# Kernel optimization log

Hardware: AMD Instinct MI355X
Metric: run time of the kernel (lower is better)

Reference implementation:

```python
import jax, jax.numpy as jnp
import numpy as np

N_NODES = 100000
N_EDGES = 1600000
N_GRAPHS = 256
IN_F = 64   # global_features (GNN input dim)
OUT_F = 64  # node_features (GNN output dim)


def setup_inputs() -> dict:
    key = jax.random.key(0)
    ks = jax.random.split(key, 8)
    x = jax.random.normal(ks[0], (N_NODES, IN_F), dtype=jnp.float32)
    edge_index = jax.random.randint(ks[1], (2, N_EDGES), 0, N_NODES, dtype=jnp.int64)
    batch = jnp.sort(jax.random.randint(ks[2], (N_NODES,), 0, N_GRAPHS, dtype=jnp.int64))
    # GNNLayer linear: in=global_features, out=node_features
    W_gnn = jax.random.normal(ks[3], (IN_F, OUT_F), dtype=jnp.float32) / np.sqrt(IN_F)
    b_gnn = jnp.zeros((OUT_F,), dtype=jnp.float32)
    # global_attention: Linear(node_features, 1)
    W_att = jax.random.normal(ks[4], (OUT_F, 1), dtype=jnp.float32) / np.sqrt(OUT_F)
    b_att = jnp.zeros((1,), dtype=jnp.float32)
    return {"x": x, "edge_index": edge_index, "batch": batch,
            "W_gnn": W_gnn, "b_gnn": b_gnn, "W_att": W_att, "b_att": b_att}


def reference(x, edge_index, batch, W_gnn, b_gnn, W_att, b_att):
    src, dst = edge_index[0], edge_index[1]
    # --- GNN message passing layer: aggregate neighbor features, transform ---
    agg = jax.ops.segment_sum(x[src], dst, num_segments=N_NODES)  # [N, IN_F]
    h = jax.nn.relu((x + agg) @ W_gnn + b_gnn)                    # [N, OUT_F]
    # --- attention scores + scatter softmax over batch segments ---
    scores = (h @ W_att + b_att)[:, 0]                            # [N]
    seg_max = jax.ops.segment_max(scores, batch, num_segments=N_GRAPHS)
    e = jnp.exp(scores - seg_max[batch])
    denom = jax.ops.segment_sum(e, batch, num_segments=N_GRAPHS)
    w = e / denom[batch]                                          # [N]
    # --- weighted scatter-add pooling ---
    out = jax.ops.segment_sum(w[:, None] * h, batch, num_segments=N_GRAPHS)
    return out  # [N_GRAPHS, OUT_F]
```

## Files before the change

kernel.cpp:

```cpp
#include <hip/hip_runtime.h>

#define N_NODES  100000
#define N_EDGES  1600000
#define N_GRAPHS 256
#define F        64


#define CHUNK    8192
#define NCHUNK   196
#define NBUCK    391
#define BCAP     5120

#define CAST_ELEMS  (N_NODES * F / 4)
#define SC_BLOCKS   2000

__device__ __forceinline__ unsigned short f2bf(float f) {
    unsigned int u = __float_as_uint(f);
    u += 0x7FFFu + ((u >> 16) & 1u);
    return (unsigned short)(u >> 16);
}
__device__ __forceinline__ float bfl(unsigned int u) { return __uint_as_float(u << 16); }
__device__ __forceinline__ float bfh(unsigned int u) { return __uint_as_float(u & 0xFFFF0000u); }

__global__ __launch_bounds__(1024) void bin_kernel(
        const int* __restrict__ src, const int* __restrict__ dst,
        unsigned int* __restrict__ pairs, int* __restrict__ balloc) {
    __shared__ int hist[NBUCK];
    __shared__ int roffs[NBUCK];
    __shared__ int curs[NBUCK];
    __shared__ int bbase[NBUCK];
    __shared__ int wsum[16];
    __shared__ unsigned int   stage[CHUNK];
    __shared__ unsigned short bstage[CHUNK];

    int tid  = threadIdx.x;
    int b    = blockIdx.x;
    int base = b * CHUNK;
    int m    = min(CHUNK, N_EDGES - base);
    int lane = tid & 63;
    int wv   = tid >> 6;

    for (int k = tid; k < NBUCK; k += 1024) hist[k] = 0;
    __syncthreads();

    int de[8], se[8];
    #pragma unroll
    for (int r = 0; r < 8; ++r) {
        int e = tid + r * 1024;
        if (e < m) {
            de[r] = dst[base + e];
            se[r] = src[base + e];
            atomicAdd(&hist[de[r] >> 8], 1);
        } else {
            de[r] = -1; se[r] = 0;
        }
    }
    __syncthreads();

    int v = (tid < NBUCK) ? hist[tid] : 0;
    #pragma unroll
    for (int o = 1; o < 64; o <<= 1) {
        int u = __shfl_up(v, o, 64);
        if (lane >= o) v += u;
    }
    if (lane == 63) wsum[wv] = v;
    __syncthreads();
    if (tid < 16) {
        int s = wsum[tid];
        #pragma unroll
        for (int o = 1; o < 16; o <<= 1) {
            int u = __shfl_up(s, o, 64);
            if (tid >= o) s += u;
        }
        wsum[tid] = s;
    }
    __syncthreads();
    if (wv > 0) v += wsum[wv - 1];
    if (tid < NBUCK) {
        int excl = v - hist[tid];
        roffs[tid] = excl;
        curs[tid]  = excl;
        if (hist[tid] > 0)
            bbase[tid] = tid * BCAP + atomicAdd(&balloc[tid], hist[tid]);
    }
    __syncthreads();

    #pragma unroll
    for (int r = 0; r < 8; ++r) {
        if (de[r] >= 0) {
            int bk  = de[r] >> 8;
            int pos = atomicAdd(&curs[bk], 1);
            stage[pos]  = ((unsigned)(de[r] & 255) << 17) | (unsigned)se[r];
            bstage[pos] = (unsigned short)bk;
        }
    }
    __syncthreads();

    for (int e = tid; e < m; e += 1024) {
        int bk = bstage[e];
        pairs[bbase[bk] + (e - roffs[bk])] = stage[e];
    }
}

__global__ __launch_bounds__(512) void sortcast_kernel(
        unsigned int* __restrict__ pairs,
        const int* __restrict__ balloc,
        int* __restrict__ nbeg, int* __restrict__ nend,
        const float* __restrict__ x, unsigned short* __restrict__ xh,
        float* __restrict__ out, float* __restrict__ denom) {
    __shared__ int hist[256];
    __shared__ int roffs[256];
    __shared__ int curs[256];
    __shared__ int wsum[8];
    __shared__ int sorted[BCAP];

    int tid = threadIdx.x;
    int b   = blockIdx.x;

    if (b >= NBUCK) {
        if (b == NBUCK) {
            for (int i = tid; i < N_GRAPHS * F; i += 512) out[i] = 0.f;
            if (tid < N_GRAPHS) denom[tid] = 0.f;
        }
        int i0      = (b - NBUCK) * 512 + tid;
        int cstride = (SC_BLOCKS - NBUCK) * 512;
        for (int i = i0; i < CAST_ELEMS; i += cstride) {
            float4 v = ((const float4*)x)[i];
            ushort4 o;
            o.x = f2bf(v.x); o.y = f2bf(v.y); o.z = f2bf(v.z); o.w = f2bf(v.w);
            ((ushort4*)xh)[i] = o;
        }
        return;
    }

    int lane  = tid & 63;
    int wv    = tid >> 6;
    int node0 = b << 8;
    int nn    = min(256, N_NODES - node0);
    int E     = balloc[b];
    int base  = b * BCAP;

    for (int k = tid; k < 256; k += 512) hist[k] = 0;
    __syncthreads();
    for (int i = tid; i < E; i += 512)
        atomicAdd(&hist[pairs[base + i] >> 17], 1);
    __syncthreads();

    int c = (tid < 256) ? hist[tid] : 0;
    int v = c;
    #pragma unroll
    for (int o = 1; o < 64; o <<= 1) {
        int u = __shfl_up(v, o, 64);
        if (lane >= o) v += u;
    }
    if (tid < 256 && lane == 63) wsum[wv] = v;
    __syncthreads();
    if (tid < 4) {
        int s = wsum[tid];
        int u = __shfl_up(s, 1, 64); if (tid >= 1) s += u;
        u     = __shfl_up(s, 2, 64); if (tid >= 2) s += u;
        wsum[tid] = s;
    }
    __syncthreads();
    if (tid < 256) {
        if (wv > 0) v += wsum[wv - 1];
        int excl = v - c;
        roffs[tid] = excl;
        curs[tid]  = excl;
        if (tid < nn) {
            nbeg[node0 + tid] = base + excl;
            nend[node0 + tid] = base + excl + c;
        }
    }
    __syncthreads();

    for (int i = tid; i < E; i += 512) {
        unsigned int p = pairs[base + i];
        int pos = atomicAdd(&curs[p >> 17], 1);
        sorted[pos] = (int)(p & 0x1FFFFu);
    }
    __syncthreads();
    for (int i = tid; i < E; i += 512)
        pairs[base + i] = (unsigned int)sorted[i];
}

#define NODES_PER_WAVE 25
#define GT_NWAVES  (N_NODES / NODES_PER_WAVE)
#define GT_BLOCKS  (GT_NWAVES / 4)

__global__ __launch_bounds__(256) void gather_pool_kernel(
        const unsigned short* __restrict__ xh,
        const int*   __restrict__ nbeg,
        const int*   __restrict__ nend,
        const int*   __restrict__ eidx,
        const int*   __restrict__ batch,
        const float* __restrict__ Wg,
        const float* __restrict__ bg,
        const float* __restrict__ Wa,
        const float* __restrict__ ba,
        float*       __restrict__ out_acc,
        float*       __restrict__ denom) {
    int tid  = threadIdx.x;
    int lane = tid & 63;
    int grp  = lane >> 3;
    int c    = lane & 7;
    int waveId = blockIdx.x * 4 + (tid >> 6);

    int n0   = waveId * NODES_PER_WAVE;
    int nEnd = n0 + NODES_PER_WAVE;

    float wcol[F];
    #pragma unroll
    for (int k = 0; k < F; ++k) wcol[k] = Wg[k * F + lane];
    float bgl = bg[lane];
    float wal = Wa[lane];
    float ba0 = ba[0];

    const uint4* xh4 = (const uint4*)xh;

    int   cur_g = batch[n0];
    float accw  = 0.f;
    float denw  = 0.f;

    int pb = nbeg[n0];
    int pe = nend[n0];
    int sl_cur = (pb + lane < pe) ? eidx[pb + lane] : 0;

    for (int n = n0; n < nEnd; ++n) {
        int start = pb, end = pe;
        int sl    = sl_cur;
        if (n + 1 < nEnd) {
            pb = nbeg[n + 1];
            pe = nend[n + 1];
            sl_cur = (pb + lane < pe) ? eidx[pb + lane] : 0;
        }

        float a0=0.f,a1=0.f,a2=0.f,a3=0.f,a4=0.f,a5=0.f,a6=0.f,a7=0.f;
        {
            int jmax = end - start; if (jmax > 64) jmax = 64;
            for (int j = 0; j < jmax; j += 8) {
                int el = j + grp;
                int s  = __shfl(sl, el, 64);
                if (el < jmax) {
                    uint4 v = xh4[s * 8 + c];
                    a0 += bfl(v.x); a1 += bfh(v.x);
                    a2 += bfl(v.y); a3 += bfh(v.y);
                    a4 += bfl(v.z); a5 += bfh(v.z);
                    a6 += bfl(v.w); a7 += bfh(v.w);
                }
            }
        }
        for (int base2 = start + 64; base2 < end; base2 += 64) {
            int jmax = end - base2; if (jmax > 64) jmax = 64;
            int sl2 = (base2 + lane < end) ? eidx[base2 + lane] : 0;
            for (int j = 0; j < jmax; j += 8) {
                int el = j + grp;
                int s  = __shfl(sl2, el, 64);
                if (el < jmax) {
                    uint4 v = xh4[s * 8 + c];
                    a0 += bfl(v.x); a1 += bfh(v.x);
                    a2 += bfl(v.y); a3 += bfh(v.y);
                    a4 += bfl(v.z); a5 += bfh(v.z);
                    a6 += bfl(v.w); a7 += bfh(v.w);
                }
            }
        }
        #pragma unroll
        for (int o = 8; o <= 32; o <<= 1) {
            a0 += __shfl_xor(a0, o, 64); a1 += __shfl_xor(a1, o, 64);
            a2 += __shfl_xor(a2, o, 64); a3 += __shfl_xor(a3, o, 64);
            a4 += __shfl_xor(a4, o, 64); a5 += __shfl_xor(a5, o, 64);
            a6 += __shfl_xor(a6, o, 64); a7 += __shfl_xor(a7, o, 64);
        }
        {
            uint4 v = xh4[n * 8 + c];
            a0 += bfl(v.x); a1 += bfh(v.x);
            a2 += bfl(v.y); a3 += bfh(v.y);
            a4 += bfl(v.z); a5 += bfh(v.z);
            a6 += bfl(v.w); a7 += bfh(v.w);
        }

        float re[8] = {a0,a1,a2,a3,a4,a5,a6,a7};
        float q0=0.f,q1=0.f,q2=0.f,q3=0.f,q4=0.f,q5=0.f,q6=0.f,q7=0.f;
        #pragma unroll
        for (int k = 0; k < F; k += 8) {
            int ln = k >> 3;
            q0 += __int_as_float(__builtin_amdgcn_readlane(__float_as_int(re[0]), ln)) * wcol[k + 0];
            q1 += __int_as_float(__builtin_amdgcn_readlane(__float_as_int(re[1]), ln)) * wcol[k + 1];
            q2 += __int_as_float(__builtin_amdgcn_readlane(__float_as_int(re[2]), ln)) * wcol[k + 2];
            q3 += __int_as_float(__builtin_amdgcn_readlane(__float_as_int(re[3]), ln)) * wcol[k + 3];
            q4 += __int_as_float(__builtin_amdgcn_readlane(__float_as_int(re[4]), ln)) * wcol[k + 4];
            q5 += __int_as_float(__builtin_amdgcn_readlane(__float_as_int(re[5]), ln)) * wcol[k + 5];
            q6 += __int_as_float(__builtin_amdgcn_readlane(__float_as_int(re[6]), ln)) * wcol[k + 6];
            q7 += __int_as_float(__builtin_amdgcn_readlane(__float_as_int(re[7]), ln)) * wcol[k + 7];
        }
        float hv = ((q0 + q1) + (q2 + q3)) + ((q4 + q5) + (q6 + q7)) + bgl;
        hv = hv > 0.f ? hv : 0.f;

        float p = hv * wal;
        #pragma unroll
        for (int o = 32; o > 0; o >>= 1)
            p += __shfl_down(p, o, 64);
        float s = __int_as_float(__builtin_amdgcn_readlane(__float_as_int(p), 0)) + ba0;
        float e = __expf(s);

        int g = batch[n];
        if (g != cur_g) {
            atomicAdd(&out_acc[cur_g * F + lane], accw);
            if (lane == 0) atomicAdd(&denom[cur_g], denw);
            accw = 0.f; denw = 0.f; cur_g = g;
        }
        accw += e * hv;
        denw += e;
    }
    atomicAdd(&out_acc[cur_g * F + lane], accw);
    if (lane == 0) atomicAdd(&denom[cur_g], denw);
}

__global__ __launch_bounds__(256) void fin_kernel(
        float* __restrict__ out, const float* __restrict__ denom) {
    int i = blockIdx.x * 256 + threadIdx.x;
    if (i >= N_GRAPHS * F) return;
    float d = denom[i >> 6];
    out[i] = (d > 0.f) ? out[i] / d : 0.f;
}

extern "C" void kernel_launch(void* const* d_in, const int* in_sizes, int n_in,
                              void* d_out, int out_size, void* d_ws, size_t ws_size,
                              hipStream_t stream) {
    const float* x     = (const float*)d_in[0];
    const int*   ei    = (const int*)d_in[1];
    const int*   batch = (const int*)d_in[2];
    const float* Wg    = (const float*)d_in[3];
    const float* bg    = (const float*)d_in[4];
    const float* Wa    = (const float*)d_in[5];
    const float* ba    = (const float*)d_in[6];
    float* out = (float*)d_out;

    const int* src = ei;
    const int* dst = ei + N_EDGES;

    char* ws = (char*)d_ws;
    unsigned short* xh     = (unsigned short*)(ws);
    unsigned int*   pairs  = (unsigned int*)(ws + 12800000);
    int*            nbeg   = (int*)(ws + 20807680);
    int*            nend   = (int*)(ws + 21207808);
    int*            balloc = (int*)(ws + 21607936);
    float*          denom  = (float*)(ws + 21610240);

    hipMemsetAsync(balloc, 0, NBUCK * sizeof(int), stream);
    bin_kernel     <<<NCHUNK, 1024, 0, stream>>>(src, dst, pairs, balloc);
    sortcast_kernel<<<SC_BLOCKS, 512, 0, stream>>>(pairs, balloc, nbeg, nend,
                                                   x, xh, out, denom);
    gather_pool_kernel<<<GT_BLOCKS, 256, 0, stream>>>(
        xh, nbeg, nend, (const int*)pairs, batch, Wg, bg, Wa, ba, out, denom);
    fin_kernel     <<<64, 256, 0, stream>>>(out, denom);
}
```

Measured before the change: 184.5 us.

## Shrink binning chunks for more blocks and fold finalize into gather kernel

The binning kernel now handles 2048-edge chunks with 512 threads across 782 blocks, where it previously used 8192-edge chunks with 1024 threads across 196 blocks. This spreads the work over more CUs and cuts per-block shared memory. The separate finalize kernel is removed: the last block of the gather/pool kernel, found with a global done counter and threadfence, divides the pooled sums by the denominators. This saves a kernel launch but adds a global atomic per block and a serial tail in one block.

```diff
diff --git a/kernel.cpp b/kernel.cpp
--- a/kernel.cpp
+++ b/kernel.cpp
@@ -6,10 +6,12 @@
 #define F        64
 
 
-#define CHUNK    8192
-#define NCHUNK   196
+#define CHUNK    2048
+#define NCHUNK   782
 #define NBUCK    391
 #define BCAP     5120
+#define BBLK     512
+#define BREPT    4
 
 #define CAST_ELEMS  (N_NODES * F / 4)
 #define SC_BLOCKS   2000
@@ -22,14 +24,14 @@
 __device__ __forceinline__ float bfl(unsigned int u) { return __uint_as_float(u << 16); }
 __device__ __forceinline__ float bfh(unsigned int u) { return __uint_as_float(u & 0xFFFF0000u); }
 
-__global__ __launch_bounds__(1024) void bin_kernel(
+__global__ __launch_bounds__(BBLK) void bin_kernel(
         const int* __restrict__ src, const int* __restrict__ dst,
         unsigned int* __restrict__ pairs, int* __restrict__ balloc) {
     __shared__ int hist[NBUCK];
     __shared__ int roffs[NBUCK];
     __shared__ int curs[NBUCK];
     __shared__ int bbase[NBUCK];
-    __shared__ int wsum[16];
+    __shared__ int wsum[8];
     __shared__ unsigned int   stage[CHUNK];
     __shared__ unsigned short bstage[CHUNK];
 
@@ -40,13 +42,13 @@
     int lane = tid & 63;
     int wv   = tid >> 6;
 
-    for (int k = tid; k < NBUCK; k += 1024) hist[k] = 0;
-    __syncthreads();
-
-    int de[8], se[8];
-    #pragma unroll
-    for (int r = 0; r < 8; ++r) {
-        int e = tid + r * 1024;
+    for (int k = tid; k < NBUCK; k += BBLK) hist[k] = 0;
+    __syncthreads();
+
+    int de[BREPT], se[BREPT];
+    #pragma unroll
+    for (int r = 0; r < BREPT; ++r) {
+        int e = tid + r * BBLK;
         if (e < m) {
             de[r] = dst[base + e];
             se[r] = src[base + e];
@@ -57,7 +59,8 @@
     }
     __syncthreads();
 
-    int v = (tid < NBUCK) ? hist[tid] : 0;
+    int cnt = (tid < NBUCK) ? hist[tid] : 0;
+    int v = cnt;
     #pragma unroll
     for (int o = 1; o < 64; o <<= 1) {
         int u = __shfl_up(v, o, 64);
@@ -65,28 +68,26 @@
     }
     if (lane == 63) wsum[wv] = v;
     __syncthreads();
-    if (tid < 16) {
+    if (tid < 8) {
         int s = wsum[tid];
-        #pragma unroll
-        for (int o = 1; o < 16; o <<= 1) {
-            int u = __shfl_up(s, o, 64);
-            if (tid >= o) s += u;
-        }
+        int u = __shfl_up(s, 1, 64); if (tid >= 1) s += u;
+        u     = __shfl_up(s, 2, 64); if (tid >= 2) s += u;
+        u     = __shfl_up(s, 4, 64); if (tid >= 4) s += u;
         wsum[tid] = s;
     }
     __syncthreads();
     if (wv > 0) v += wsum[wv - 1];
     if (tid < NBUCK) {
-        int excl = v - hist[tid];
+        int excl = v - cnt;
         roffs[tid] = excl;
         curs[tid]  = excl;
-        if (hist[tid] > 0)
-            bbase[tid] = tid * BCAP + atomicAdd(&balloc[tid], hist[tid]);
-    }
-    __syncthreads();
-
-    #pragma unroll
-    for (int r = 0; r < 8; ++r) {
+        if (cnt > 0)
+            bbase[tid] = tid * BCAP + atomicAdd(&balloc[tid], cnt);
+    }
+    __syncthreads();
+
+    #pragma unroll
+    for (int r = 0; r < BREPT; ++r) {
         if (de[r] >= 0) {
             int bk  = de[r] >> 8;
             int pos = atomicAdd(&curs[bk], 1);
@@ -96,7 +97,7 @@
     }
     __syncthreads();
 
-    for (int e = tid; e < m; e += 1024) {
+    for (int e = tid; e < m; e += BBLK) {
         int bk = bstage[e];
         pairs[bbase[bk] + (e - roffs[bk])] = stage[e];
     }
@@ -199,7 +200,9 @@
         const float* __restrict__ Wa,
         const float* __restrict__ ba,
         float*       __restrict__ out_acc,
-        float*       __restrict__ denom) {
+        float*       __restrict__ denom,
+        unsigned int* __restrict__ done) {
+    __shared__ int lastFlag;
     int tid  = threadIdx.x;
     int lane = tid & 63;
     int grp  = lane >> 3;
@@ -315,14 +318,23 @@
     }
     atomicAdd(&out_acc[cur_g * F + lane], accw);
     if (lane == 0) atomicAdd(&denom[cur_g], denw);
-}
-
-__global__ __launch_bounds__(256) void fin_kernel(
-        float* __restrict__ out, const float* __restrict__ denom) {
-    int i = blockIdx.x * 256 + threadIdx.x;
-    if (i >= N_GRAPHS * F) return;
-    float d = denom[i >> 6];
-    out[i] = (d > 0.f) ? out[i] / d : 0.f;
+
+    __threadfence();
+    __syncthreads();
+    if (tid == 0) {
+        unsigned int prev = atomicAdd(done, 1u);
+        lastFlag = (prev == (unsigned)(gridDim.x - 1)) ? 1 : 0;
+    }
+    __syncthreads();
+    if (lastFlag) {
+        for (int i = tid; i < N_GRAPHS * F; i += 256) {
+            float d = __hip_atomic_load(&denom[i >> 6], __ATOMIC_RELAXED,
+                                        __HIP_MEMORY_SCOPE_AGENT);
+            float o = __hip_atomic_load(&out_acc[i], __ATOMIC_RELAXED,
+                                        __HIP_MEMORY_SCOPE_AGENT);
+            out_acc[i] = (d > 0.f) ? o / d : 0.f;
+        }
+    }
 }
 
 extern "C" void kernel_launch(void* const* d_in, const int* in_sizes, int n_in,
@@ -346,13 +358,14 @@
     int*            nbeg   = (int*)(ws + 20807680);
     int*            nend   = (int*)(ws + 21207808);
     int*            balloc = (int*)(ws + 21607936);
+    unsigned int*   done   = (unsigned int*)(ws + 21609984);
     float*          denom  = (float*)(ws + 21610240);
 
-    hipMemsetAsync(balloc, 0, NBUCK * sizeof(int), stream);
-    bin_kernel     <<<NCHUNK, 1024, 0, stream>>>(src, dst, pairs, balloc);
+    hipMemsetAsync(balloc, 0, 2048 + 256, stream);
+    bin_kernel     <<<NCHUNK, BBLK, 0, stream>>>(src, dst, pairs, balloc);
     sortcast_kernel<<<SC_BLOCKS, 512, 0, stream>>>(pairs, balloc, nbeg, nend,
                                                    x, xh, out, denom);
     gather_pool_kernel<<<GT_BLOCKS, 256, 0, stream>>>(
-        xh, nbeg, nend, (const int*)pairs, batch, Wg, bg, Wa, ba, out, denom);
-    fin_kernel     <<<64, 256, 0, stream>>>(out, denom);
-}
+        xh, nbeg, nend, (const int*)pairs, batch, Wg, bg, Wa, ba,
+        out, denom, done);
+}
```

New measurement: 297.8 us. 1.61x slower.
